# Kernel optimization log

Hardware: AMD Instinct MI355X
Metric: run time of the kernel (lower is better)

The kernel has to match this reference:

```python
import jax, jax.numpy as jnp
import numpy as np

SE_TEMP = 0.2
BN_EPS = 1e-5

def _l2n(x):
    # F.normalize(p=2, dim=-1) with eps=1e-12 clamp on the norm
    n = jnp.linalg.norm(x, axis=-1, keepdims=True)
    return x / jnp.maximum(n, 1e-12)

def setup_inputs() -> dict:
    key = jax.random.key(0)
    k1, k2, k3, k4, k5 = jax.random.split(key, 5)
    Q, I, D = 256, 2048, 256
    return {
        "query_feats": jax.random.normal(k1, (Q, D), dtype=jnp.float32),
        "query_img_feats": jax.random.normal(k2, (Q, D), dtype=jnp.float32),
        "gallery_img_feats": jax.random.normal(k3, (I, D), dtype=jnp.float32),
        "bn_gamma": jnp.ones((D,), dtype=jnp.float32),
        "bn_beta": jnp.zeros((D,), dtype=jnp.float32),
        "bn_mean": jax.random.normal(k4, (D,), dtype=jnp.float32) * 0.1,
        "bn_var": jax.random.uniform(k5, (D,), dtype=jnp.float32, minval=0.5, maxval=1.5),
    }

def reference(query_feats, query_img_feats, gallery_img_feats, bn_gamma, bn_beta, bn_mean, bn_var):
    # GalleryFilterNetwork.get_scores, mode='combined', gfn_activation_mode='se'
    inv_std = bn_gamma / jnp.sqrt(bn_var + BN_EPS)

    def bn(x):  # eval-mode BatchNorm1d over last dim D
        return (x - bn_mean) * inv_std + bn_beta

    xq = _l2n(query_feats)        # [Q, D] normalized query box feats
    yq = _l2n(query_img_feats)    # [Q, D] normalized query scene feats
    yg = _l2n(gallery_img_feats)  # [I, D] normalized gallery scene feats

    gate = jax.nn.sigmoid(xq / SE_TEMP)           # [Q, D]
    fused_query = bn(yq * gate)                   # [Q, D]  (non-p SE fuse)
    fused_gal = bn(yg[:, None, :] * gate[None])   # [I, Q, D] (p=True SE fuse)

    # cosine similarity per (q, i) pair, then sigmoid
    scores = jax.nn.sigmoid(
        jnp.einsum('qd,iqd->qi', _l2n(fused_query), _l2n(fused_gal))
    )
    return scores  # [Q, I]
```

## Files before the change

kernel.cpp:

```cpp
#include <hip/hip_runtime.h>
#include <math.h>

#define D 256
#define Q 256
#define I 2048

typedef __attribute__((ext_vector_type(8))) short short8;
typedef __attribute__((ext_vector_type(4))) float floatx4;

__device__ __forceinline__ float wave_sum(float v) {
#pragma unroll
    for (int off = 1; off < 64; off <<= 1)
        v += __shfl_xor(v, off, 64);
    return v;
}

__device__ __forceinline__ float sigmoidf_(float x) {
    return 1.0f / (1.0f + expf(-x));
}

__device__ __forceinline__ unsigned short f2bf(float f) {
    unsigned u = __float_as_uint(f);
    u += 0x7FFFu + ((u >> 16) & 1u);
    return (unsigned short)(u >> 16);
}

__global__ void __launch_bounds__(256)
prep_all(const float* __restrict__ qf,
         const float* __restrict__ qif,
         const float* __restrict__ gal,
         const float* __restrict__ gamma,
         const float* __restrict__ beta,
         const float* __restrict__ mean,
         const float* __restrict__ var,
         unsigned short* __restrict__ PB,
         unsigned short* __restrict__ WB,
         unsigned short* __restrict__ VB,
         unsigned short* __restrict__ YB,
         unsigned short* __restrict__ Y2B,
         float* __restrict__ sq,
         float* __restrict__ ccp) {
    const int t = threadIdx.x;
    const int wv = t >> 6;
    const int l  = t & 63;

    if (blockIdx.x < 64) {
        const int i0 = blockIdx.x * 32;
        const float4* g4 = (const float4*)gal;
#pragma unroll
        for (int r = 0; r < 8; r++) {
            const int row = i0 + wv * 8 + r;
            float4 x = g4[(size_t)row * 64 + l];
            float s = wave_sum(x.x * x.x + x.y * x.y + x.z * x.z + x.w * x.w);
            float inv = 1.0f / fmaxf(sqrtf(s), 1e-12f);
            float y0 = x.x * inv, y1 = x.y * inv, y2 = x.z * inv, y3 = x.w * inv;
            *(ushort4*)&YB[(size_t)row * D + 4 * l] =
                make_ushort4(f2bf(y0), f2bf(y1), f2bf(y2), f2bf(y3));
            *(ushort4*)&Y2B[(size_t)row * D + 4 * l] =
                make_ushort4(f2bf(y0 * y0), f2bf(y1 * y1),
                             f2bf(y2 * y2), f2bf(y3 * y3));
        }
    } else {
        const int q = (blockIdx.x - 64) * 4 + wv;
        const float4* qf4  = (const float4*)qf;
        const float4* qif4 = (const float4*)qif;
        const float4* ga4  = (const float4*)gamma;
        const float4* be4  = (const float4*)beta;
        const float4* me4  = (const float4*)mean;
        const float4* va4  = (const float4*)var;

        float4 x = qf4[(size_t)q * 64 + l];
        float nx = wave_sum(x.x * x.x + x.y * x.y + x.z * x.z + x.w * x.w);
        float inx = 1.0f / fmaxf(sqrtf(nx), 1e-12f);
        float g0 = sigmoidf_(x.x * inx * 5.0f);
        float g1 = sigmoidf_(x.y * inx * 5.0f);
        float g2 = sigmoidf_(x.z * inx * 5.0f);
        float g3 = sigmoidf_(x.w * inx * 5.0f);

        float4 y = qif4[(size_t)q * 64 + l];
        float ny = wave_sum(y.x * y.x + y.y * y.y + y.z * y.z + y.w * y.w);
        float iny = 1.0f / fmaxf(sqrtf(ny), 1e-12f);

        float4 gm = ga4[l], bt = be4[l], mn = me4[l], vr = va4[l];
        float is0 = gm.x * rsqrtf(vr.x + 1e-5f);
        float is1 = gm.y * rsqrtf(vr.y + 1e-5f);
        float is2 = gm.z * rsqrtf(vr.z + 1e-5f);
        float is3 = gm.w * rsqrtf(vr.w + 1e-5f);
        float c0 = bt.x - mn.x * is0;
        float c1 = bt.y - mn.y * is1;
        float c2 = bt.z - mn.z * is2;
        float c3 = bt.w - mn.w * is3;
        float a0 = g0 * is0, a1 = g1 * is1, a2 = g2 * is2, a3 = g3 * is3;

        float f0 = y.x * iny * a0 + c0;
        float f1 = y.y * iny * a1 + c1;
        float f2 = y.z * iny * a2 + c2;
        float f3 = y.w * iny * a3 + c3;
        float nf = wave_sum(f0 * f0 + f1 * f1 + f2 * f2 + f3 * f3);
        float inf_ = 1.0f / fmaxf(sqrtf(nf), 1e-12f);
        float u0 = f0 * inf_, u1 = f1 * inf_, u2 = f2 * inf_, u3 = f3 * inf_;

        *(ushort4*)&PB[(size_t)q * D + 4 * l] =
            make_ushort4(f2bf(u0 * a0), f2bf(u1 * a1),
                         f2bf(u2 * a2), f2bf(u3 * a3));
        *(ushort4*)&WB[(size_t)q * D + 4 * l] =
            make_ushort4(f2bf(a0 * a0), f2bf(a1 * a1),
                         f2bf(a2 * a2), f2bf(a3 * a3));
        *(ushort4*)&VB[(size_t)q * D + 4 * l] =
            make_ushort4(f2bf(2.0f * a0 * c0), f2bf(2.0f * a1 * c1),
                         f2bf(2.0f * a2 * c2), f2bf(2.0f * a3 * c3));

        float s = wave_sum(u0 * c0 + u1 * c1 + u2 * c2 + u3 * c3);
        if (l == 0) sq[q] = s;

        if (q == 0) {
            float ccs = wave_sum(c0 * c0 + c1 * c1 + c2 * c2 + c3 * c3);
            if (l == 0) *ccp = ccs;
        }
    }
}

__global__ void __launch_bounds__(256)
main_scores(const unsigned short* __restrict__ YB,
            const unsigned short* __restrict__ Y2B,
            const unsigned short* __restrict__ PB,
            const unsigned short* __restrict__ WB,
            const unsigned short* __restrict__ VB,
            const float* __restrict__ sq,
            const float* __restrict__ ccp,
            float* __restrict__ out) {
    const int t = threadIdx.x, wv = t >> 6, l = t & 63;
    const int lm = l & 15, quad = l >> 4;
    const int q0 = blockIdx.x * 64 + wv * 16;
    const int qr = q0 + lm;
    const int koff = quad * 8;

    short8 bp[8], bw[8], bv[8];
#pragma unroll
    for (int ks = 0; ks < 8; ks++) {
        const size_t o = (size_t)qr * D + ks * 32 + koff;
        bp[ks] = *(const short8*)&PB[o];
        bw[ks] = *(const short8*)&WB[o];
        bv[ks] = *(const short8*)&VB[o];
    }
    const float sqv = sq[qr];
    const float ccv = *ccp;

#pragma unroll
    for (int it = 0; it < 2; it++) {
        const int i_t = blockIdx.y * 32 + it * 16;
        const int ir = i_t + lm;
        floatx4 acc1 = {0.f, 0.f, 0.f, 0.f};
        floatx4 acc2 = {0.f, 0.f, 0.f, 0.f};
#pragma unroll
        for (int ks = 0; ks < 8; ks++) {
            const size_t o = (size_t)ir * D + ks * 32 + koff;
            short8 ay  = *(const short8*)&YB[o];
            short8 ay2 = *(const short8*)&Y2B[o];
            acc1 = __builtin_amdgcn_mfma_f32_16x16x32_bf16(ay,  bp[ks], acc1, 0, 0, 0);
            acc2 = __builtin_amdgcn_mfma_f32_16x16x32_bf16(ay2, bw[ks], acc2, 0, 0, 0);
            acc2 = __builtin_amdgcn_mfma_f32_16x16x32_bf16(ay,  bv[ks], acc2, 0, 0, 0);
        }
        float4 o4;
        float* po = &o4.x;
#pragma unroll
        for (int r = 0; r < 4; r++) {
            float nrm = fmaxf(sqrtf(fmaxf(acc2[r] + ccv, 0.f)), 1e-12f);
            po[r] = sigmoidf_((acc1[r] + sqv) / nrm);
        }
        *(float4*)&out[(size_t)qr * I + i_t + quad * 4] = o4;
    }
}

extern "C" void kernel_launch(void* const* d_in, const int* in_sizes, int n_in,
                              void* d_out, int out_size, void* d_ws, size_t ws_size,
                              hipStream_t stream) {
    const float* qf    = (const float*)d_in[0];
    const float* qif   = (const float*)d_in[1];
    const float* gal   = (const float*)d_in[2];
    const float* gamma = (const float*)d_in[3];
    const float* beta  = (const float*)d_in[4];
    const float* mean  = (const float*)d_in[5];
    const float* var   = (const float*)d_in[6];
    float* out = (float*)d_out;

    char* base = (char*)d_ws;
    float* sq = (float*)base;
    float* cc = (float*)(base + 1024);
    unsigned short* PB  = (unsigned short*)(base + 2048);
    unsigned short* WB  = PB + (size_t)Q * D;
    unsigned short* VB  = WB + (size_t)Q * D;
    unsigned short* YB  = VB + (size_t)Q * D;
    unsigned short* Y2B = YB + (size_t)I * D;

    prep_all<<<128, 256, 0, stream>>>(qf, qif, gal, gamma, beta, mean, var,
                                      PB, WB, VB, YB, Y2B, sq, cc);
    main_scores<<<dim3(Q / 64, I / 32), 256, 0, stream>>>(YB, Y2B, PB, WB, VB,
                                                          sq, cc, out);
}
```

Baseline: 78.25 us.

## Fuse prep and score kernels into one with LDS-staged bf16 operands

Merges the normalization/gating prep kernel into the MFMA scoring kernel, so each block computes its own query and gallery bf16 operands directly into padded shared memory. This removes the second launch and the global workspace write/read round trip. In exchange, query preprocessing (including sigmoids) is recomputed redundantly by every gallery block, and the large LDS footprint limits occupancy to one block per CU.

```diff
diff --git a/kernel.cpp b/kernel.cpp
--- a/kernel.cpp
+++ b/kernel.cpp
@@ -4,14 +4,16 @@
 #define D 256
 #define Q 256
 #define I 2048
+#define STRIDE 264
 
 typedef __attribute__((ext_vector_type(8))) short short8;
 typedef __attribute__((ext_vector_type(4))) float floatx4;
 
-__device__ __forceinline__ float wave_sum(float v) {
-#pragma unroll
-    for (int off = 1; off < 64; off <<= 1)
-        v += __shfl_xor(v, off, 64);
+__device__ __forceinline__ float grp16_sum(float v) {
+    v += __shfl_xor(v, 1, 64);
+    v += __shfl_xor(v, 2, 64);
+    v += __shfl_xor(v, 4, 64);
+    v += __shfl_xor(v, 8, 64);
     return v;
 }
 
@@ -25,138 +27,168 @@
     return (unsigned short)(u >> 16);
 }
 
-__global__ void __launch_bounds__(256)
-prep_all(const float* __restrict__ qf,
-         const float* __restrict__ qif,
-         const float* __restrict__ gal,
-         const float* __restrict__ gamma,
-         const float* __restrict__ beta,
-         const float* __restrict__ mean,
-         const float* __restrict__ var,
-         unsigned short* __restrict__ PB,
-         unsigned short* __restrict__ WB,
-         unsigned short* __restrict__ VB,
-         unsigned short* __restrict__ YB,
-         unsigned short* __restrict__ Y2B,
-         float* __restrict__ sq,
-         float* __restrict__ ccp) {
-    const int t = threadIdx.x;
-    const int wv = t >> 6;
-    const int l  = t & 63;
-
-    if (blockIdx.x < 64) {
-        const int i0 = blockIdx.x * 32;
-        const float4* g4 = (const float4*)gal;
-#pragma unroll
-        for (int r = 0; r < 8; r++) {
-            const int row = i0 + wv * 8 + r;
-            float4 x = g4[(size_t)row * 64 + l];
-            float s = wave_sum(x.x * x.x + x.y * x.y + x.z * x.z + x.w * x.w);
-            float inv = 1.0f / fmaxf(sqrtf(s), 1e-12f);
-            float y0 = x.x * inv, y1 = x.y * inv, y2 = x.z * inv, y3 = x.w * inv;
-            *(ushort4*)&YB[(size_t)row * D + 4 * l] =
-                make_ushort4(f2bf(y0), f2bf(y1), f2bf(y2), f2bf(y3));
-            *(ushort4*)&Y2B[(size_t)row * D + 4 * l] =
-                make_ushort4(f2bf(y0 * y0), f2bf(y1 * y1),
-                             f2bf(y2 * y2), f2bf(y3 * y3));
-        }
-    } else {
-        const int q = (blockIdx.x - 64) * 4 + wv;
-        const float4* qf4  = (const float4*)qf;
-        const float4* qif4 = (const float4*)qif;
-        const float4* ga4  = (const float4*)gamma;
-        const float4* be4  = (const float4*)beta;
-        const float4* me4  = (const float4*)mean;
-        const float4* va4  = (const float4*)var;
-
-        float4 x = qf4[(size_t)q * 64 + l];
-        float nx = wave_sum(x.x * x.x + x.y * x.y + x.z * x.z + x.w * x.w);
-        float inx = 1.0f / fmaxf(sqrtf(nx), 1e-12f);
-        float g0 = sigmoidf_(x.x * inx * 5.0f);
-        float g1 = sigmoidf_(x.y * inx * 5.0f);
-        float g2 = sigmoidf_(x.z * inx * 5.0f);
-        float g3 = sigmoidf_(x.w * inx * 5.0f);
-
-        float4 y = qif4[(size_t)q * 64 + l];
-        float ny = wave_sum(y.x * y.x + y.y * y.y + y.z * y.z + y.w * y.w);
-        float iny = 1.0f / fmaxf(sqrtf(ny), 1e-12f);
-
-        float4 gm = ga4[l], bt = be4[l], mn = me4[l], vr = va4[l];
-        float is0 = gm.x * rsqrtf(vr.x + 1e-5f);
-        float is1 = gm.y * rsqrtf(vr.y + 1e-5f);
-        float is2 = gm.z * rsqrtf(vr.z + 1e-5f);
-        float is3 = gm.w * rsqrtf(vr.w + 1e-5f);
-        float c0 = bt.x - mn.x * is0;
-        float c1 = bt.y - mn.y * is1;
-        float c2 = bt.z - mn.z * is2;
-        float c3 = bt.w - mn.w * is3;
-        float a0 = g0 * is0, a1 = g1 * is1, a2 = g2 * is2, a3 = g3 * is3;
-
-        float f0 = y.x * iny * a0 + c0;
-        float f1 = y.y * iny * a1 + c1;
-        float f2 = y.z * iny * a2 + c2;
-        float f3 = y.w * iny * a3 + c3;
-        float nf = wave_sum(f0 * f0 + f1 * f1 + f2 * f2 + f3 * f3);
-        float inf_ = 1.0f / fmaxf(sqrtf(nf), 1e-12f);
-        float u0 = f0 * inf_, u1 = f1 * inf_, u2 = f2 * inf_, u3 = f3 * inf_;
-
-        *(ushort4*)&PB[(size_t)q * D + 4 * l] =
-            make_ushort4(f2bf(u0 * a0), f2bf(u1 * a1),
-                         f2bf(u2 * a2), f2bf(u3 * a3));
-        *(ushort4*)&WB[(size_t)q * D + 4 * l] =
-            make_ushort4(f2bf(a0 * a0), f2bf(a1 * a1),
-                         f2bf(a2 * a2), f2bf(a3 * a3));
-        *(ushort4*)&VB[(size_t)q * D + 4 * l] =
-            make_ushort4(f2bf(2.0f * a0 * c0), f2bf(2.0f * a1 * c1),
-                         f2bf(2.0f * a2 * c2), f2bf(2.0f * a3 * c3));
-
-        float s = wave_sum(u0 * c0 + u1 * c1 + u2 * c2 + u3 * c3);
-        if (l == 0) sq[q] = s;
-
-        if (q == 0) {
-            float ccs = wave_sum(c0 * c0 + c1 * c1 + c2 * c2 + c3 * c3);
-            if (l == 0) *ccp = ccs;
-        }
-    }
-}
-
-__global__ void __launch_bounds__(256)
-main_scores(const unsigned short* __restrict__ YB,
-            const unsigned short* __restrict__ Y2B,
-            const unsigned short* __restrict__ PB,
-            const unsigned short* __restrict__ WB,
-            const unsigned short* __restrict__ VB,
-            const float* __restrict__ sq,
-            const float* __restrict__ ccp,
-            float* __restrict__ out) {
+__global__ void __launch_bounds__(256, 1)
+fused_scores(const float* __restrict__ qf,
+             const float* __restrict__ qif,
+             const float* __restrict__ gal,
+             const float* __restrict__ gamma,
+             const float* __restrict__ beta,
+             const float* __restrict__ mean,
+             const float* __restrict__ var,
+             float* __restrict__ out) {
+    __shared__ unsigned short sP[64 * STRIDE];
+    __shared__ unsigned short sW[64 * STRIDE];
+    __shared__ unsigned short sV[64 * STRIDE];
+    __shared__ unsigned short sY[32 * STRIDE];
+    __shared__ unsigned short sY2[32 * STRIDE];
+    __shared__ float ssq[64];
+
     const int t = threadIdx.x, wv = t >> 6, l = t & 63;
-    const int lm = l & 15, quad = l >> 4;
-    const int q0 = blockIdx.x * 64 + wv * 16;
-    const int qr = q0 + lm;
-    const int koff = quad * 8;
-
+    const int jq = l >> 4, s = l & 15;
+    const int q0 = blockIdx.x * 64, i0 = blockIdx.y * 32;
+
+    const float4* ga4 = (const float4*)gamma;
+    const float4* be4 = (const float4*)beta;
+    const float4* me4 = (const float4*)mean;
+    const float4* va4 = (const float4*)var;
+    float isv[16], cv[16];
+#pragma unroll
+    for (int m = 0; m < 4; m++) {
+        float4 gm = ga4[s * 4 + m], vr = va4[s * 4 + m];
+        float4 bt = be4[s * 4 + m], mn = me4[s * 4 + m];
+        isv[4 * m + 0] = gm.x * rsqrtf(vr.x + 1e-5f);
+        isv[4 * m + 1] = gm.y * rsqrtf(vr.y + 1e-5f);
+        isv[4 * m + 2] = gm.z * rsqrtf(vr.z + 1e-5f);
+        isv[4 * m + 3] = gm.w * rsqrtf(vr.w + 1e-5f);
+        cv[4 * m + 0] = bt.x - mn.x * isv[4 * m + 0];
+        cv[4 * m + 1] = bt.y - mn.y * isv[4 * m + 1];
+        cv[4 * m + 2] = bt.z - mn.z * isv[4 * m + 2];
+        cv[4 * m + 3] = bt.w - mn.w * isv[4 * m + 3];
+    }
+    float ccl = 0.f;
+#pragma unroll
+    for (int e = 0; e < 16; e++) ccl += cv[e] * cv[e];
+    const float cc = grp16_sum(ccl);
+
+    const float4* g4 = (const float4*)gal;
+    float gx[2][16];
+#pragma unroll
+    for (int rr = 0; rr < 2; rr++) {
+        const int i = i0 + wv * 8 + rr * 4 + jq;
+#pragma unroll
+        for (int m = 0; m < 4; m++) {
+            float4 r = g4[(size_t)i * 64 + s * 4 + m];
+            gx[rr][4 * m + 0] = r.x; gx[rr][4 * m + 1] = r.y;
+            gx[rr][4 * m + 2] = r.z; gx[rr][4 * m + 3] = r.w;
+        }
+    }
+#pragma unroll
+    for (int rr = 0; rr < 2; rr++) {
+        const int iloc = wv * 8 + rr * 4 + jq;
+        float nn = 0.f;
+#pragma unroll
+        for (int e = 0; e < 16; e++) nn += gx[rr][e] * gx[rr][e];
+        nn = grp16_sum(nn);
+        const float inv = 1.0f / fmaxf(sqrtf(nn), 1e-12f);
+        unsigned short uy[16], uy2[16];
+#pragma unroll
+        for (int e = 0; e < 16; e++) {
+            float y = gx[rr][e] * inv;
+            uy[e]  = f2bf(y);
+            uy2[e] = f2bf(y * y);
+        }
+        *(short8*)&sY [iloc * STRIDE + s * 16]     = *(short8*)&uy[0];
+        *(short8*)&sY [iloc * STRIDE + s * 16 + 8] = *(short8*)&uy[8];
+        *(short8*)&sY2[iloc * STRIDE + s * 16]     = *(short8*)&uy2[0];
+        *(short8*)&sY2[iloc * STRIDE + s * 16 + 8] = *(short8*)&uy2[8];
+    }
+
+    const float4* qf4 = (const float4*)qf;
+    const float4* qi4 = (const float4*)qif;
+    float qx[4][16], qy[4][16];
+#pragma unroll
+    for (int r = 0; r < 4; r++) {
+        const int q = q0 + wv * 16 + r * 4 + jq;
+#pragma unroll
+        for (int m = 0; m < 4; m++) {
+            float4 a = qf4[(size_t)q * 64 + s * 4 + m];
+            float4 b = qi4[(size_t)q * 64 + s * 4 + m];
+            qx[r][4 * m + 0] = a.x; qx[r][4 * m + 1] = a.y;
+            qx[r][4 * m + 2] = a.z; qx[r][4 * m + 3] = a.w;
+            qy[r][4 * m + 0] = b.x; qy[r][4 * m + 1] = b.y;
+            qy[r][4 * m + 2] = b.z; qy[r][4 * m + 3] = b.w;
+        }
+    }
+#pragma unroll
+    for (int r = 0; r < 4; r++) {
+        const int qloc = wv * 16 + r * 4 + jq;
+        float nx = 0.f, ny = 0.f;
+#pragma unroll
+        for (int e = 0; e < 16; e++) {
+            nx += qx[r][e] * qx[r][e];
+            ny += qy[r][e] * qy[r][e];
+        }
+        nx = grp16_sum(nx);
+        ny = grp16_sum(ny);
+        const float inx = 1.0f / fmaxf(sqrtf(nx), 1e-12f);
+        const float iny = 1.0f / fmaxf(sqrtf(ny), 1e-12f);
+
+        float av[16], fv[16];
+        float nf = 0.f;
+#pragma unroll
+        for (int e = 0; e < 16; e++) {
+            float gate = sigmoidf_(qx[r][e] * inx * 5.0f);
+            av[e] = gate * isv[e];
+            fv[e] = qy[r][e] * iny * av[e] + cv[e];
+            nf += fv[e] * fv[e];
+        }
+        nf = grp16_sum(nf);
+        const float inf_ = 1.0f / fmaxf(sqrtf(nf), 1e-12f);
+
+        unsigned short up[16], uw[16], uv[16];
+        float usum = 0.f;
+#pragma unroll
+        for (int e = 0; e < 16; e++) {
+            float u = fv[e] * inf_;
+            up[e] = f2bf(u * av[e]);
+            uw[e] = f2bf(av[e] * av[e]);
+            uv[e] = f2bf(2.0f * av[e] * cv[e]);
+            usum += u * cv[e];
+        }
+        usum = grp16_sum(usum);
+        if (s == 0) ssq[qloc] = usum;
+
+        *(short8*)&sP[qloc * STRIDE + s * 16]     = *(short8*)&up[0];
+        *(short8*)&sP[qloc * STRIDE + s * 16 + 8] = *(short8*)&up[8];
+        *(short8*)&sW[qloc * STRIDE + s * 16]     = *(short8*)&uw[0];
+        *(short8*)&sW[qloc * STRIDE + s * 16 + 8] = *(short8*)&uw[8];
+        *(short8*)&sV[qloc * STRIDE + s * 16]     = *(short8*)&uv[0];
+        *(short8*)&sV[qloc * STRIDE + s * 16 + 8] = *(short8*)&uv[8];
+    }
+
+    __syncthreads();
+
+    const int lm = l & 15, quad = l >> 4, koff = quad * 8;
     short8 bp[8], bw[8], bv[8];
 #pragma unroll
     for (int ks = 0; ks < 8; ks++) {
-        const size_t o = (size_t)qr * D + ks * 32 + koff;
-        bp[ks] = *(const short8*)&PB[o];
-        bw[ks] = *(const short8*)&WB[o];
-        bv[ks] = *(const short8*)&VB[o];
-    }
-    const float sqv = sq[qr];
-    const float ccv = *ccp;
+        const int o = (wv * 16 + lm) * STRIDE + ks * 32 + koff;
+        bp[ks] = *(const short8*)&sP[o];
+        bw[ks] = *(const short8*)&sW[o];
+        bv[ks] = *(const short8*)&sV[o];
+    }
+    const float sqv = ssq[wv * 16 + lm];
+    const int qr = q0 + wv * 16 + lm;
 
 #pragma unroll
     for (int it = 0; it < 2; it++) {
-        const int i_t = blockIdx.y * 32 + it * 16;
-        const int ir = i_t + lm;
         floatx4 acc1 = {0.f, 0.f, 0.f, 0.f};
         floatx4 acc2 = {0.f, 0.f, 0.f, 0.f};
 #pragma unroll
         for (int ks = 0; ks < 8; ks++) {
-            const size_t o = (size_t)ir * D + ks * 32 + koff;
-            short8 ay  = *(const short8*)&YB[o];
-            short8 ay2 = *(const short8*)&Y2B[o];
+            const int o = (it * 16 + lm) * STRIDE + ks * 32 + koff;
+            short8 ay  = *(const short8*)&sY[o];
+            short8 ay2 = *(const short8*)&sY2[o];
             acc1 = __builtin_amdgcn_mfma_f32_16x16x32_bf16(ay,  bp[ks], acc1, 0, 0, 0);
             acc2 = __builtin_amdgcn_mfma_f32_16x16x32_bf16(ay2, bw[ks], acc2, 0, 0, 0);
             acc2 = __builtin_amdgcn_mfma_f32_16x16x32_bf16(ay,  bv[ks], acc2, 0, 0, 0);
@@ -164,11 +196,11 @@
         float4 o4;
         float* po = &o4.x;
 #pragma unroll
-        for (int r = 0; r < 4; r++) {
-            float nrm = fmaxf(sqrtf(fmaxf(acc2[r] + ccv, 0.f)), 1e-12f);
-            po[r] = sigmoidf_((acc1[r] + sqv) / nrm);
-        }
-        *(float4*)&out[(size_t)qr * I + i_t + quad * 4] = o4;
+        for (int rr = 0; rr < 4; rr++) {
+            float nrm = fmaxf(sqrtf(fmaxf(acc2[rr] + cc, 0.f)), 1e-12f);
+            po[rr] = sigmoidf_((acc1[rr] + sqv) / nrm);
+        }
+        *(float4*)&out[(size_t)qr * I + i0 + it * 16 + quad * 4] = o4;
     }
 }
 
@@ -184,17 +216,6 @@
     const float* var   = (const float*)d_in[6];
     float* out = (float*)d_out;
 
-    char* base = (char*)d_ws;
-    float* sq = (float*)base;
-    float* cc = (float*)(base + 1024);
-    unsigned short* PB  = (unsigned short*)(base + 2048);
-    unsigned short* WB  = PB + (size_t)Q * D;
-    unsigned short* VB  = WB + (size_t)Q * D;
-    unsigned short* YB  = VB + (size_t)Q * D;
-    unsigned short* Y2B = YB + (size_t)I * D;
-
-    prep_all<<<128, 256, 0, stream>>>(qf, qif, gal, gamma, beta, mean, var,
-                                      PB, WB, VB, YB, Y2B, sq, cc);
-    main_scores<<<dim3(Q / 64, I / 32), 256, 0, stream>>>(YB, Y2B, PB, WB, VB,
-                                                          sq, cc, out);
-}
+    fused_scores<<<dim3(Q / 64, I / 32), 256, 0, stream>>>(
+        qf, qif, gal, gamma, beta, mean, var, out);
+}
```

Result: slower. 80.70 us (+3.1%).

## Fuse gallery normalization into score kernel via padded LDS tiles

Applied to the files above, without the earlier changes.

Gallery rows are no longer normalized into global bf16 buffers by the prep kernel. Each score block now loads its 32 fp32 gallery rows, normalizes them and converts y and y² to bf16, and stages both in padded shared memory that the MFMA loop reads. This drops the global write and re-read of YB/Y2B and shrinks the prep kernel to the query-only work. In exchange, each gallery row is normalized redundantly by the 4 q-blocks that use it, and fp32 gallery data is read four times instead of bf16.

```diff
diff --git a/kernel.cpp b/kernel.cpp
--- a/kernel.cpp
+++ b/kernel.cpp
@@ -4,6 +4,7 @@
 #define D 256
 #define Q 256
 #define I 2048
+#define STRIDE 264
 
 typedef __attribute__((ext_vector_type(8))) short short8;
 typedef __attribute__((ext_vector_type(4))) float floatx4;
@@ -12,6 +13,14 @@
 #pragma unroll
     for (int off = 1; off < 64; off <<= 1)
         v += __shfl_xor(v, off, 64);
+    return v;
+}
+
+__device__ __forceinline__ float grp16_sum(float v) {
+    v += __shfl_xor(v, 1, 64);
+    v += __shfl_xor(v, 2, 64);
+    v += __shfl_xor(v, 4, 64);
+    v += __shfl_xor(v, 8, 64);
     return v;
 }
 
@@ -26,115 +35,125 @@
 }
 
 __global__ void __launch_bounds__(256)
-prep_all(const float* __restrict__ qf,
-         const float* __restrict__ qif,
-         const float* __restrict__ gal,
-         const float* __restrict__ gamma,
-         const float* __restrict__ beta,
-         const float* __restrict__ mean,
-         const float* __restrict__ var,
-         unsigned short* __restrict__ PB,
-         unsigned short* __restrict__ WB,
-         unsigned short* __restrict__ VB,
-         unsigned short* __restrict__ YB,
-         unsigned short* __restrict__ Y2B,
-         float* __restrict__ sq,
-         float* __restrict__ ccp) {
+query_prep(const float* __restrict__ qf,
+           const float* __restrict__ qif,
+           const float* __restrict__ gamma,
+           const float* __restrict__ beta,
+           const float* __restrict__ mean,
+           const float* __restrict__ var,
+           unsigned short* __restrict__ PB,
+           unsigned short* __restrict__ WB,
+           unsigned short* __restrict__ VB,
+           float* __restrict__ sq,
+           float* __restrict__ ccp) {
     const int t = threadIdx.x;
-    const int wv = t >> 6;
-    const int l  = t & 63;
-
-    if (blockIdx.x < 64) {
-        const int i0 = blockIdx.x * 32;
-        const float4* g4 = (const float4*)gal;
-#pragma unroll
-        for (int r = 0; r < 8; r++) {
-            const int row = i0 + wv * 8 + r;
-            float4 x = g4[(size_t)row * 64 + l];
-            float s = wave_sum(x.x * x.x + x.y * x.y + x.z * x.z + x.w * x.w);
-            float inv = 1.0f / fmaxf(sqrtf(s), 1e-12f);
-            float y0 = x.x * inv, y1 = x.y * inv, y2 = x.z * inv, y3 = x.w * inv;
-            *(ushort4*)&YB[(size_t)row * D + 4 * l] =
-                make_ushort4(f2bf(y0), f2bf(y1), f2bf(y2), f2bf(y3));
-            *(ushort4*)&Y2B[(size_t)row * D + 4 * l] =
-                make_ushort4(f2bf(y0 * y0), f2bf(y1 * y1),
-                             f2bf(y2 * y2), f2bf(y3 * y3));
-        }
-    } else {
-        const int q = (blockIdx.x - 64) * 4 + wv;
-        const float4* qf4  = (const float4*)qf;
-        const float4* qif4 = (const float4*)qif;
-        const float4* ga4  = (const float4*)gamma;
-        const float4* be4  = (const float4*)beta;
-        const float4* me4  = (const float4*)mean;
-        const float4* va4  = (const float4*)var;
-
-        float4 x = qf4[(size_t)q * 64 + l];
-        float nx = wave_sum(x.x * x.x + x.y * x.y + x.z * x.z + x.w * x.w);
-        float inx = 1.0f / fmaxf(sqrtf(nx), 1e-12f);
-        float g0 = sigmoidf_(x.x * inx * 5.0f);
-        float g1 = sigmoidf_(x.y * inx * 5.0f);
-        float g2 = sigmoidf_(x.z * inx * 5.0f);
-        float g3 = sigmoidf_(x.w * inx * 5.0f);
-
-        float4 y = qif4[(size_t)q * 64 + l];
-        float ny = wave_sum(y.x * y.x + y.y * y.y + y.z * y.z + y.w * y.w);
-        float iny = 1.0f / fmaxf(sqrtf(ny), 1e-12f);
-
-        float4 gm = ga4[l], bt = be4[l], mn = me4[l], vr = va4[l];
-        float is0 = gm.x * rsqrtf(vr.x + 1e-5f);
-        float is1 = gm.y * rsqrtf(vr.y + 1e-5f);
-        float is2 = gm.z * rsqrtf(vr.z + 1e-5f);
-        float is3 = gm.w * rsqrtf(vr.w + 1e-5f);
-        float c0 = bt.x - mn.x * is0;
-        float c1 = bt.y - mn.y * is1;
-        float c2 = bt.z - mn.z * is2;
-        float c3 = bt.w - mn.w * is3;
-        float a0 = g0 * is0, a1 = g1 * is1, a2 = g2 * is2, a3 = g3 * is3;
-
-        float f0 = y.x * iny * a0 + c0;
-        float f1 = y.y * iny * a1 + c1;
-        float f2 = y.z * iny * a2 + c2;
-        float f3 = y.w * iny * a3 + c3;
-        float nf = wave_sum(f0 * f0 + f1 * f1 + f2 * f2 + f3 * f3);
-        float inf_ = 1.0f / fmaxf(sqrtf(nf), 1e-12f);
-        float u0 = f0 * inf_, u1 = f1 * inf_, u2 = f2 * inf_, u3 = f3 * inf_;
-
-        *(ushort4*)&PB[(size_t)q * D + 4 * l] =
-            make_ushort4(f2bf(u0 * a0), f2bf(u1 * a1),
-                         f2bf(u2 * a2), f2bf(u3 * a3));
-        *(ushort4*)&WB[(size_t)q * D + 4 * l] =
-            make_ushort4(f2bf(a0 * a0), f2bf(a1 * a1),
-                         f2bf(a2 * a2), f2bf(a3 * a3));
-        *(ushort4*)&VB[(size_t)q * D + 4 * l] =
-            make_ushort4(f2bf(2.0f * a0 * c0), f2bf(2.0f * a1 * c1),
-                         f2bf(2.0f * a2 * c2), f2bf(2.0f * a3 * c3));
-
-        float s = wave_sum(u0 * c0 + u1 * c1 + u2 * c2 + u3 * c3);
-        if (l == 0) sq[q] = s;
-
-        if (q == 0) {
-            float ccs = wave_sum(c0 * c0 + c1 * c1 + c2 * c2 + c3 * c3);
-            if (l == 0) *ccp = ccs;
-        }
+    const int wv = t >> 6, l = t & 63;
+    const int q = blockIdx.x * 4 + wv;
+    const float4* qf4  = (const float4*)qf;
+    const float4* qif4 = (const float4*)qif;
+    const float4* ga4  = (const float4*)gamma;
+    const float4* be4  = (const float4*)beta;
+    const float4* me4  = (const float4*)mean;
+    const float4* va4  = (const float4*)var;
+
+    float4 x = qf4[(size_t)q * 64 + l];
+    float nx = wave_sum(x.x * x.x + x.y * x.y + x.z * x.z + x.w * x.w);
+    float inx = 1.0f / fmaxf(sqrtf(nx), 1e-12f);
+    float g0 = sigmoidf_(x.x * inx * 5.0f);
+    float g1 = sigmoidf_(x.y * inx * 5.0f);
+    float g2 = sigmoidf_(x.z * inx * 5.0f);
+    float g3 = sigmoidf_(x.w * inx * 5.0f);
+
+    float4 y = qif4[(size_t)q * 64 + l];
+    float ny = wave_sum(y.x * y.x + y.y * y.y + y.z * y.z + y.w * y.w);
+    float iny = 1.0f / fmaxf(sqrtf(ny), 1e-12f);
+
+    float4 gm = ga4[l], bt = be4[l], mn = me4[l], vr = va4[l];
+    float is0 = gm.x * rsqrtf(vr.x + 1e-5f);
+    float is1 = gm.y * rsqrtf(vr.y + 1e-5f);
+    float is2 = gm.z * rsqrtf(vr.z + 1e-5f);
+    float is3 = gm.w * rsqrtf(vr.w + 1e-5f);
+    float c0 = bt.x - mn.x * is0;
+    float c1 = bt.y - mn.y * is1;
+    float c2 = bt.z - mn.z * is2;
+    float c3 = bt.w - mn.w * is3;
+    float a0 = g0 * is0, a1 = g1 * is1, a2 = g2 * is2, a3 = g3 * is3;
+
+    float f0 = y.x * iny * a0 + c0;
+    float f1 = y.y * iny * a1 + c1;
+    float f2 = y.z * iny * a2 + c2;
+    float f3 = y.w * iny * a3 + c3;
+    float nf = wave_sum(f0 * f0 + f1 * f1 + f2 * f2 + f3 * f3);
+    float inf_ = 1.0f / fmaxf(sqrtf(nf), 1e-12f);
+    float u0 = f0 * inf_, u1 = f1 * inf_, u2 = f2 * inf_, u3 = f3 * inf_;
+
+    *(ushort4*)&PB[(size_t)q * D + 4 * l] =
+        make_ushort4(f2bf(u0 * a0), f2bf(u1 * a1), f2bf(u2 * a2), f2bf(u3 * a3));
+    *(ushort4*)&WB[(size_t)q * D + 4 * l] =
+        make_ushort4(f2bf(a0 * a0), f2bf(a1 * a1), f2bf(a2 * a2), f2bf(a3 * a3));
+    *(ushort4*)&VB[(size_t)q * D + 4 * l] =
+        make_ushort4(f2bf(2.0f * a0 * c0), f2bf(2.0f * a1 * c1),
+                     f2bf(2.0f * a2 * c2), f2bf(2.0f * a3 * c3));
+
+    float s = wave_sum(u0 * c0 + u1 * c1 + u2 * c2 + u3 * c3);
+    if (l == 0) sq[q] = s;
+
+    if (q == 0) {
+        float ccs = wave_sum(c0 * c0 + c1 * c1 + c2 * c2 + c3 * c3);
+        if (l == 0) *ccp = ccs;
     }
 }
 
 __global__ void __launch_bounds__(256)
-main_scores(const unsigned short* __restrict__ YB,
-            const unsigned short* __restrict__ Y2B,
+main_scores(const float* __restrict__ gal,
             const unsigned short* __restrict__ PB,
             const unsigned short* __restrict__ WB,
             const unsigned short* __restrict__ VB,
             const float* __restrict__ sq,
             const float* __restrict__ ccp,
             float* __restrict__ out) {
+    __shared__ unsigned short sY[32 * STRIDE];
+    __shared__ unsigned short sY2[32 * STRIDE];
+
     const int t = threadIdx.x, wv = t >> 6, l = t & 63;
-    const int lm = l & 15, quad = l >> 4;
-    const int q0 = blockIdx.x * 64 + wv * 16;
-    const int qr = q0 + lm;
-    const int koff = quad * 8;
-
+    const int jq = l >> 4, s = l & 15;
+    const int q0 = blockIdx.x * 64, i0 = blockIdx.y * 32;
+
+    const float4* g4 = (const float4*)gal;
+    float gx[2][16];
+#pragma unroll
+    for (int rr = 0; rr < 2; rr++) {
+        const int i = i0 + wv * 8 + rr * 4 + jq;
+#pragma unroll
+        for (int m = 0; m < 4; m++) {
+            float4 r = g4[(size_t)i * 64 + s * 4 + m];
+            gx[rr][4 * m + 0] = r.x; gx[rr][4 * m + 1] = r.y;
+            gx[rr][4 * m + 2] = r.z; gx[rr][4 * m + 3] = r.w;
+        }
+    }
+#pragma unroll
+    for (int rr = 0; rr < 2; rr++) {
+        const int iloc = wv * 8 + rr * 4 + jq;
+        float nn = 0.f;
+#pragma unroll
+        for (int e = 0; e < 16; e++) nn += gx[rr][e] * gx[rr][e];
+        nn = grp16_sum(nn);
+        const float inv = 1.0f / fmaxf(sqrtf(nn), 1e-12f);
+        unsigned short uy[16], uy2[16];
+#pragma unroll
+        for (int e = 0; e < 16; e++) {
+            float yv = gx[rr][e] * inv;
+            uy[e]  = f2bf(yv);
+            uy2[e] = f2bf(yv * yv);
+        }
+        *(short8*)&sY [iloc * STRIDE + s * 16]     = *(short8*)&uy[0];
+        *(short8*)&sY [iloc * STRIDE + s * 16 + 8] = *(short8*)&uy[8];
+        *(short8*)&sY2[iloc * STRIDE + s * 16]     = *(short8*)&uy2[0];
+        *(short8*)&sY2[iloc * STRIDE + s * 16 + 8] = *(short8*)&uy2[8];
+    }
+
+    const int lm = l & 15, quad = l >> 4, koff = quad * 8;
+    const int qr = q0 + wv * 16 + lm;
     short8 bp[8], bw[8], bv[8];
 #pragma unroll
     for (int ks = 0; ks < 8; ks++) {
@@ -146,17 +165,17 @@
     const float sqv = sq[qr];
     const float ccv = *ccp;
 
+    __syncthreads();
+
 #pragma unroll
     for (int it = 0; it < 2; it++) {
-        const int i_t = blockIdx.y * 32 + it * 16;
-        const int ir = i_t + lm;
         floatx4 acc1 = {0.f, 0.f, 0.f, 0.f};
         floatx4 acc2 = {0.f, 0.f, 0.f, 0.f};
 #pragma unroll
         for (int ks = 0; ks < 8; ks++) {
-            const size_t o = (size_t)ir * D + ks * 32 + koff;
-            short8 ay  = *(const short8*)&YB[o];
-            short8 ay2 = *(const short8*)&Y2B[o];
+            const int o = (it * 16 + lm) * STRIDE + ks * 32 + koff;
+            short8 ay  = *(const short8*)&sY[o];
+            short8 ay2 = *(const short8*)&sY2[o];
             acc1 = __builtin_amdgcn_mfma_f32_16x16x32_bf16(ay,  bp[ks], acc1, 0, 0, 0);
             acc2 = __builtin_amdgcn_mfma_f32_16x16x32_bf16(ay2, bw[ks], acc2, 0, 0, 0);
             acc2 = __builtin_amdgcn_mfma_f32_16x16x32_bf16(ay,  bv[ks], acc2, 0, 0, 0);
@@ -164,11 +183,11 @@
         float4 o4;
         float* po = &o4.x;
 #pragma unroll
-        for (int r = 0; r < 4; r++) {
-            float nrm = fmaxf(sqrtf(fmaxf(acc2[r] + ccv, 0.f)), 1e-12f);
-            po[r] = sigmoidf_((acc1[r] + sqv) / nrm);
-        }
-        *(float4*)&out[(size_t)qr * I + i_t + quad * 4] = o4;
+        for (int rr = 0; rr < 4; rr++) {
+            float nrm = fmaxf(sqrtf(fmaxf(acc2[rr] + ccv, 0.f)), 1e-12f);
+            po[rr] = sigmoidf_((acc1[rr] + sqv) / nrm);
+        }
+        *(float4*)&out[(size_t)qr * I + i0 + it * 16 + quad * 4] = o4;
     }
 }
 
@@ -187,14 +206,12 @@
     char* base = (char*)d_ws;
     float* sq = (float*)base;
     float* cc = (float*)(base + 1024);
-    unsigned short* PB  = (unsigned short*)(base + 2048);
-    unsigned short* WB  = PB + (size_t)Q * D;
-    unsigned short* VB  = WB + (size_t)Q * D;
-    unsigned short* YB  = VB + (size_t)Q * D;
-    unsigned short* Y2B = YB + (size_t)I * D;
-
-    prep_all<<<128, 256, 0, stream>>>(qf, qif, gal, gamma, beta, mean, var,
-                                      PB, WB, VB, YB, Y2B, sq, cc);
-    main_scores<<<dim3(Q / 64, I / 32), 256, 0, stream>>>(YB, Y2B, PB, WB, VB,
+    unsigned short* PB = (unsigned short*)(base + 2048);
+    unsigned short* WB = PB + (size_t)Q * D;
+    unsigned short* VB = WB + (size_t)Q * D;
+
+    query_prep<<<Q / 4, 256, 0, stream>>>(qf, qif, gamma, beta, mean, var,
+                                          PB, WB, VB, sq, cc);
+    main_scores<<<dim3(Q / 64, I / 32), 256, 0, stream>>>(gal, PB, WB, VB,
                                                           sq, cc, out);
 }
```

After: 75.61 us. 3.4% less time.
